# Performance work log

Measured on AMD Instinct MI355X. Metric: run time of the kernel, lower is better.

Reference implementation:

```python
import jax, jax.numpy as jnp
import numpy as np

AB = 8            # activation quant bits
NOISE_LEVEL = 0.1
CY_SCALE = 2.0    # stands in for args.cy_scale
B, IN, H = 8192, 512, 512


def _fake_quant(x, bits, sign):
    # forward: clip/clamp then round-to-grid; backward (STE) handled elsewhere
    if sign:
        delta = 1.0 / (2.0 ** (bits - 1))
        xc = jnp.clip(x, -1.0 + delta, 1.0 - delta)
        scale = 2.0 ** (bits - 1)
    else:
        xc = jnp.clip(x, 0.0, 1.0)
        scale = 2.0 ** bits
    q = jnp.round(xc * scale) / scale
    # STE: identity gradient w.r.t. x
    return x + jax.lax.stop_gradient(q - x)


def setup_inputs() -> dict:
    key = jax.random.key(0)
    ks = jax.random.split(key, 11)
    return {
        "input": jax.random.normal(ks[0], (B, IN), jnp.float32),
        "hx": jax.random.normal(ks[1], (B, H), jnp.float32),
        "cx": jax.random.normal(ks[2], (B, H), jnp.float32),
        "weight_ih": jax.random.normal(ks[3], (4 * H, IN), jnp.float32),
        "weight_hh": jax.random.normal(ks[4], (4 * H, H), jnp.float32),
        "bias_ih": jax.random.normal(ks[5], (4 * H,), jnp.float32),
        "bias_hh": jax.random.normal(ks[6], (4 * H,), jnp.float32),
        "noise_ih": jax.random.normal(ks[7], (IN, 4 * H), jnp.float32),
        "noise_hh": jax.random.normal(ks[8], (H, 4 * H), jnp.float32),
        "noise_bias_ih": jax.random.normal(ks[9], (4 * H,), jnp.float32),
        "noise_bias_hh": jax.random.normal(ks[10], (4 * H,), jnp.float32),
    }


def reference(input, hx, cx, weight_ih, weight_hh, bias_ih, bias_hh,
              noise_ih, noise_hh, noise_bias_ih, noise_bias_hh):
    # noisy weights: noise = randn * w.max() * noise_level (raw randn passed in)
    w_ih = weight_ih.T + noise_ih * (jnp.max(weight_ih) * NOISE_LEVEL)   # [IN,4H]
    w_hh = weight_hh.T + noise_hh * (jnp.max(weight_hh) * NOISE_LEVEL)   # [H,4H]
    b_ih = bias_ih + noise_bias_ih * (jnp.max(bias_ih) * NOISE_LEVEL)
    b_hh = bias_hh + noise_bias_hh * (jnp.max(bias_hh) * NOISE_LEVEL)

    gates = input @ w_ih + b_ih + hx @ w_hh + b_hh                        # [B,4H]
    ingate, forgetgate, cellgate, outgate = jnp.split(gates, 4, axis=1)

    ingate = _fake_quant(jax.nn.sigmoid(ingate), AB, False)
    forgetgate = _fake_quant(jax.nn.sigmoid(forgetgate), AB, False)
    cellgate = _fake_quant(jnp.tanh(cellgate), AB, True)
    outgate = _fake_quant(jax.nn.sigmoid(outgate), AB, False)

    cy = _fake_quant(
        (_fake_quant(forgetgate * cx, AB, True)
         + _fake_quant(ingate * cellgate, AB, True)) / CY_SCALE,
        AB, True)
    hy = _fake_quant(
        outgate * _fake_quant(jnp.tanh(cy * CY_SCALE), AB, True),
        AB, True)
    return (hy, cy)
```

## Files before the change

### kernel.cpp

```cpp
#include <hip/hip_runtime.h>
#include <cstdint>

typedef unsigned short u16;
typedef __bf16 bf16x8 __attribute__((ext_vector_type(8)));
typedef float f32x4 __attribute__((ext_vector_type(4)));

#define NB 8192
#define HD 512
#define KD 1024
#define ND 2048
#define HY_OFF (NB * HD)
#define NT 32

__device__ __forceinline__ u16 f2bf(float f) {
  unsigned u = __float_as_uint(f);
  u += 0x7FFFu + ((u >> 16) & 1u);
  return (u16)(u >> 16);
}
__device__ __forceinline__ float bf2f(u16 h) {
  return __uint_as_float(((unsigned)h) << 16);
}
__device__ __forceinline__ void atomicMaxF(float* a, float v) {
  if (v >= 0.f) atomicMax((int*)a, __float_as_int(v));
  else          atomicMin((unsigned int*)a, __float_as_uint(v));
}
__device__ __forceinline__ float fq_u(float x) {
  float xc = fminf(fmaxf(x, 0.0f), 1.0f);
  return rintf(xc * 256.0f) * (1.0f / 256.0f);
}
__device__ __forceinline__ float fq_s(float x) {
  const float lim = 1.0f - 1.0f / 128.0f;
  float xc = fminf(fmaxf(x, -lim), lim);
  return rintf(xc * 128.0f) * (1.0f / 128.0f);
}
__device__ __forceinline__ float sigm(float x) { return 1.0f / (1.0f + expf(-x)); }

__device__ __forceinline__ void gload_lds16(const u16* g, u16* l) {
  __builtin_amdgcn_global_load_lds(
      (const __attribute__((address_space(1))) void*)g,
      (__attribute__((address_space(3))) void*)l, 16, 0, 0);
}

__global__ __launch_bounds__(256) void k_prep_max(
    const float* __restrict__ w_ih, const float* __restrict__ w_hh,
    const float* __restrict__ b_ih, const float* __restrict__ b_hh,
    float* __restrict__ maxes) {
  int bid = blockIdx.x;
  const float* src; int slot, base;
  if (bid < 1024)      { src = w_ih; slot = 0; base = bid * 1024; }
  else if (bid < 2048) { src = w_hh; slot = 1; base = (bid - 1024) * 1024; }
  else if (bid < 2050) { src = b_ih; slot = 2; base = (bid - 2048) * 1024; }
  else                 { src = b_hh; slot = 3; base = (bid - 2050) * 1024; }
  float m = -INFINITY;
  for (int i = threadIdx.x; i < 1024; i += 256) m = fmaxf(m, src[base + i]);
  for (int k = 1; k < 64; k <<= 1) m = fmaxf(m, __shfl_xor(m, k, 64));
  __shared__ float sm[4];
  if ((threadIdx.x & 63) == 0) sm[threadIdx.x >> 6] = m;
  __syncthreads();
  if (threadIdx.x == 0) {
    m = fmaxf(fmaxf(sm[0], sm[1]), fmaxf(sm[2], sm[3]));
    atomicMaxF(&maxes[slot], m);
  }
}

__global__ __launch_bounds__(256) void k_prep_build(
    const float* __restrict__ input, const float* __restrict__ hx,
    const float* __restrict__ w_ih, const float* __restrict__ w_hh,
    const float* __restrict__ n_ih, const float* __restrict__ n_hh,
    const float* __restrict__ b_ih, const float* __restrict__ b_hh,
    const float* __restrict__ nb_ih, const float* __restrict__ nb_hh,
    const float* __restrict__ maxes,
    u16* __restrict__ Xhi, u16* __restrict__ Xlo,
    u16* __restrict__ Whi, u16* __restrict__ Wlo,
    float* __restrict__ biasC) {
  const int bid = blockIdx.x;
  if (bid < 2048) {
    const int total4 = NB * KD / 4;
    for (int e4 = bid * 256 + threadIdx.x; e4 < total4; e4 += 2048 * 256) {
      int row = e4 >> 8;
      int c4  = e4 & 255;
      float4 v = (c4 < 128)
          ? reinterpret_cast<const float4*>(input)[row * 128 + c4]
          : reinterpret_cast<const float4*>(hx)[row * 128 + (c4 - 128)];
      float xs[4] = {v.x, v.y, v.z, v.w};
      ushort4 hi, lo;
      u16 h0 = f2bf(xs[0]); u16 l0 = f2bf(xs[0] - bf2f(h0));
      u16 h1 = f2bf(xs[1]); u16 l1 = f2bf(xs[1] - bf2f(h1));
      u16 h2 = f2bf(xs[2]); u16 l2 = f2bf(xs[2] - bf2f(h2));
      u16 h3 = f2bf(xs[3]); u16 l3 = f2bf(xs[3] - bf2f(h3));
      hi.x = h0; hi.y = h1; hi.z = h2; hi.w = h3;
      lo.x = l0; lo.y = l1; lo.z = l2; lo.w = l3;
      reinterpret_cast<ushort4*>(Xhi)[e4] = hi;
      reinterpret_cast<ushort4*>(Xlo)[e4] = lo;
    }
  } else if (bid < 2560) {
    __shared__ float nT[256][17];
    const int w  = bid - 2048;
    const int cg = w >> 2, kb = w & 3;
    const int j0 = cg * 16;
    const int g  = ((j0 >> 7) & 1) * 2 + ((j0 >> 4) & 1);
    const int hb = ((j0 >> 8) << 2) | ((j0 >> 5) & 3);
    const int col0 = g * 512 + (hb << 4);
    const int k0 = kb * 256;
    {
      const int cl = threadIdx.x & 15;
      const int kr = threadIdx.x >> 4;
#pragma unroll 4
      for (int i = 0; i < 16; ++i) {
        const int k = k0 + kr + 16 * i;
        nT[kr + 16 * i][cl] = (k < 512) ? n_ih[k * ND + col0 + cl]
                                        : n_hh[(k - 512) * ND + col0 + cl];
      }
    }
    __syncthreads();
    const float s_ih = maxes[0] * 0.1f, s_hh = maxes[1] * 0.1f;
    const int c  = threadIdx.x >> 4;
    const int kl = threadIdx.x & 15;
    const int colL = col0 + c;
    const int j = j0 + c;
#pragma unroll
    for (int kk = 0; kk < 4; ++kk) {
      const int k = k0 + kk * 64 + kl * 4;
      float4 wv; float s;
      if (k < 512) {
        wv = reinterpret_cast<const float4*>(w_ih)[(colL * 512 + k) >> 2];
        s = s_ih;
      } else {
        wv = reinterpret_cast<const float4*>(w_hh)[(colL * 512 + k - 512) >> 2];
        s = s_hh;
      }
      const int kt = k - k0;
      float xs[4] = {wv.x + nT[kt + 0][c] * s, wv.y + nT[kt + 1][c] * s,
                     wv.z + nT[kt + 2][c] * s, wv.w + nT[kt + 3][c] * s};
      ushort4 hi, lo;
      u16 h0 = f2bf(xs[0]); u16 l0 = f2bf(xs[0] - bf2f(h0));
      u16 h1 = f2bf(xs[1]); u16 l1 = f2bf(xs[1] - bf2f(h1));
      u16 h2 = f2bf(xs[2]); u16 l2 = f2bf(xs[2] - bf2f(h2));
      u16 h3 = f2bf(xs[3]); u16 l3 = f2bf(xs[3] - bf2f(h3));
      hi.x = h0; hi.y = h1; hi.z = h2; hi.w = h3;
      lo.x = l0; lo.y = l1; lo.z = l2; lo.w = l3;
      reinterpret_cast<ushort4*>(Whi)[(j * KD + k) >> 2] = hi;
      reinterpret_cast<ushort4*>(Wlo)[(j * KD + k) >> 2] = lo;
    }
  } else {
    int j = (bid - 2560) * 256 + threadIdx.x;
    if (j < ND) {
      int g  = ((j >> 7) & 1) * 2 + ((j >> 4) & 1);
      int hb = ((j >> 8) << 2) | ((j >> 5) & 3);
      int col = g * 512 + (hb << 4) + (j & 15);
      biasC[j] = b_ih[col] + nb_ih[col] * (maxes[2] * 0.1f)
               + b_hh[col] + nb_hh[col] * (maxes[3] * 0.1f);
    }
  }
}

__global__ __launch_bounds__(512, 2) void k_gemm_lstm(
    const u16* __restrict__ Xhi, const u16* __restrict__ Xlo,
    const u16* __restrict__ Whi, const u16* __restrict__ Wlo,
    const float* __restrict__ biasC, const float* __restrict__ cx,
    float* __restrict__ out) {
  __shared__ u16 L[2][4][8192];
  const int tid  = threadIdx.x;
  const int lane = tid & 63, wid = tid >> 6;
  const int wr = wid >> 2, wc = wid & 3;
  const int lr = lane & 15, lg = lane >> 4;
  const int xcd = blockIdx.x & 7, tt = blockIdx.x >> 3;
  const int bm = ((xcd >> 1) << 3) | (tt & 7);
  const int bn = ((xcd & 1) << 2) | (tt >> 3);
  const int mbase = bm * 256, nbase = bn * 256;

  const int l8 = lane >> 3, l7 = lane & 7;
  const int csrc  = l7 ^ l8;
  const int srow  = wid * 16 + 2 * l8 + (csrc >> 2);
  const int skoff = (csrc & 3) * 8;
  const int sdst  = wid * 512;

  const int fro = (lr >> 1) * 64 + ((((lr & 1) << 2) | lg) ^ ((lr >> 1) & 7)) * 8;

  f32x4 acc[8][4] = {};
  bf16x8 afr[4][2];
  bf16x8 bfr[2][2][2];

#define STAGE(V, SLOT, BUF, HALF)                                             \
  {                                                                           \
    const u16* arr_ = (BUF) == 0 ? Xhi : (BUF) == 1 ? Xlo                     \
                      : (BUF) == 2 ? Whi : Wlo;                               \
    const int gb_ = ((BUF) < 2 ? mbase : nbase) + (HALF) * 128 + srow;        \
    gload_lds16(arr_ + (size_t)gb_ * KD + (V) * 32 + skoff,                   \
                &L[(SLOT)][(BUF)][(HALF) * 4096 + sdst]);                     \
  }

#define PH(S, MH, NH, LOADA, LOADB, STAGE_CODE, WAIT_CODE)                    \
  {                                                                           \
    if (LOADA) {                                                              \
      _Pragma("unroll") for (int m2 = 0; m2 < 4; ++m2) {                      \
        const int ab = ((MH) * 128 + wr * 64 + m2 * 16) * 32 + fro;           \
        afr[m2][0] = *reinterpret_cast<const bf16x8*>(&L[S][0][ab]);          \
        afr[m2][1] = *reinterpret_cast<const bf16x8*>(&L[S][1][ab]);          \
      }                                                                       \
    }                                                                         \
    if (LOADB) {                                                              \
      _Pragma("unroll") for (int n2 = 0; n2 < 2; ++n2) {                      \
        const int bb = ((NH) * 128 + wc * 32 + n2 * 16) * 32 + fro;           \
        bfr[(NH)][n2][0] = *reinterpret_cast<const bf16x8*>(&L[S][2][bb]);    \
        bfr[(NH)][n2][1] = *reinterpret_cast<const bf16x8*>(&L[S][3][bb]);    \
      }                                                                       \
    }                                                                         \
    STAGE_CODE;                                                               \
    WAIT_CODE;                                                                \
    __builtin_amdgcn_s_barrier();                                             \
    __builtin_amdgcn_s_setprio(1);                                            \
    _Pragma("unroll") for (int t = 0; t < 3; ++t)                             \
      _Pragma("unroll") for (int m2 = 0; m2 < 4; ++m2)                        \
        _Pragma("unroll") for (int n2 = 0; n2 < 2; ++n2) {                    \
          f32x4* ac = &acc[(MH) * 4 + m2][(NH) * 2 + n2];                     \
          *ac = __builtin_amdgcn_mfma_f32_16x16x32_bf16(afr[m2][t == 1],      \
                    bfr[(NH)][n2][t == 2], *ac, 0, 0, 0);                     \
        }                                                                     \
    __builtin_amdgcn_s_setprio(0);                                            \
    __builtin_amdgcn_s_barrier();                                             \
  }

#define V6 asm volatile("s_waitcnt vmcnt(6)" ::: "memory")
#define V0 asm volatile("s_waitcnt vmcnt(0)" ::: "memory")

#define TILE(U, S)                                                            \
  PH(S, 0, 0, 1, 1,                                                           \
     { STAGE((U) + 1, (S) ^ 1, 0, 1); STAGE((U) + 1, (S) ^ 1, 1, 1); }, )     \
  PH(S, 0, 1, 0, 1,                                                           \
     { STAGE((U) + 2, (S), 0, 0); STAGE((U) + 2, (S), 1, 0); }, )             \
  PH(S, 1, 1, 1, 0,                                                           \
     { STAGE((U) + 2, (S), 2, 0); STAGE((U) + 2, (S), 3, 0); }, )             \
  PH(S, 1, 0, 0, 0,                                                           \
     { STAGE((U) + 2, (S), 2, 1); STAGE((U) + 2, (S), 3, 1); }, V6)

  STAGE(0, 0, 0, 0); STAGE(0, 0, 1, 0);
  STAGE(0, 0, 2, 0); STAGE(0, 0, 3, 0);
  STAGE(0, 0, 2, 1); STAGE(0, 0, 3, 1);
  STAGE(0, 0, 0, 1); STAGE(0, 0, 1, 1);
  STAGE(1, 1, 0, 0); STAGE(1, 1, 1, 0);
  STAGE(1, 1, 2, 0); STAGE(1, 1, 3, 0);
  STAGE(1, 1, 2, 1); STAGE(1, 1, 3, 1);
  V6;
  __builtin_amdgcn_s_barrier();

  for (int u = 0; u < NT - 4; u += 2) {
    TILE(u, 0)
    TILE(u + 1, 1)
  }
  TILE(NT - 4, 0)
  TILE(NT - 3, 1)
  PH(0, 0, 0, 1, 1, { STAGE(31, 1, 0, 1); STAGE(31, 1, 1, 1); }, )
  PH(0, 0, 1, 0, 1, , )
  PH(0, 1, 1, 1, 0, , )
  PH(0, 1, 0, 0, 0, , V0)
  PH(1, 0, 0, 1, 1, , )
  PH(1, 0, 1, 0, 1, , )
  PH(1, 1, 1, 1, 0, , )
  PH(1, 1, 0, 0, 0, , )

#undef TILE
#undef V6
#undef V0
#undef PH
#undef STAGE

  const int hb = bn * 4 + wc;
  const int h = hb * 16 + lr;
  float bias[4];
#pragma unroll
  for (int g = 0; g < 4; ++g)
    bias[g] = biasC[bn * 256 + ((g >> 1) * 8 + wc * 2 + (g & 1)) * 16 + lr];
#pragma unroll
  for (int mh = 0; mh < 2; ++mh) {
#pragma unroll
    for (int m2 = 0; m2 < 4; ++m2) {
      const int m = mh * 4 + m2;
#pragma unroll
      for (int r = 0; r < 4; ++r) {
        const int row = mbase + mh * 128 + wr * 64 + m2 * 16 + lg * 4 + r;
        const float gi = acc[m][0][r] + bias[0];
        const float gf = acc[m][1][r] + bias[1];
        const float gc = acc[m][2][r] + bias[2];
        const float go = acc[m][3][r] + bias[3];
        const float ig = fq_u(sigm(gi));
        const float fg = fq_u(sigm(gf));
        const float cg = fq_s(tanhf(gc));
        const float og = fq_u(sigm(go));
        const float cxv = cx[(size_t)row * HD + h];
        const float t1 = fq_s(fg * cxv);
        const float t2 = fq_s(ig * cg);
        const float cyv = fq_s((t1 + t2) * 0.5f);
        const float hyv = fq_s(og * fq_s(tanhf(cyv * 2.0f)));
        out[(size_t)row * HD + h] = hyv;
        out[HY_OFF + (size_t)row * HD + h] = cyv;
      }
    }
  }
}

extern "C" void kernel_launch(void* const* d_in, const int* in_sizes, int n_in,
                              void* d_out, int out_size, void* d_ws, size_t ws_size,
                              hipStream_t stream) {
  const float* input = (const float*)d_in[0];
  const float* hx    = (const float*)d_in[1];
  const float* cx    = (const float*)d_in[2];
  const float* w_ih  = (const float*)d_in[3];
  const float* w_hh  = (const float*)d_in[4];
  const float* b_ih  = (const float*)d_in[5];
  const float* b_hh  = (const float*)d_in[6];
  const float* n_ih  = (const float*)d_in[7];
  const float* n_hh  = (const float*)d_in[8];
  const float* nb_ih = (const float*)d_in[9];
  const float* nb_hh = (const float*)d_in[10];
  float* out = (float*)d_out;

  char* ws = (char*)d_ws;
  float* maxes = (float*)ws;
  u16* Xhi = (u16*)(ws + 256);
  u16* Xlo = (u16*)(ws + 256 + 16777216);
  u16* Whi = (u16*)(ws + 256 + 2 * 16777216);
  u16* Wlo = (u16*)(ws + 256 + 2 * 16777216 + 4194304);
  float* biasC = (float*)(ws + 256 + 2 * 16777216 + 2 * 4194304);

  hipMemsetAsync(maxes, 0xFF, 16, stream);
  hipLaunchKernelGGL(k_prep_max, dim3(2052), dim3(256), 0, stream,
                     w_ih, w_hh, b_ih, b_hh, maxes);
  hipLaunchKernelGGL(k_prep_build, dim3(2568), dim3(256), 0, stream,
                     input, hx, w_ih, w_hh, n_ih, n_hh, b_ih, b_hh,
                     nb_ih, nb_hh, maxes, Xhi, Xlo, Whi, Wlo, biasC);
  hipLaunchKernelGGL(k_gemm_lstm, dim3(256), dim3(512), 0, stream,
                     Xhi, Xlo, Whi, Wlo, biasC, cx, out);
}
```

Measured before the change: 146.4 us.

## Double-buffer LDS fragment registers to prefetch next phase operands during MFMA

Splits the A/B register fragments into two ping-pong sets and issues LDS reads for the next phase's operands (including the next K-tile's A half) before the barrier of the current phase, so LDS read latency overlaps with MFMA work. Adds sched_barrier fences to keep the compiler from reordering, moves the vmcnt wait to a different phase with a tighter count, and restructures the loop tail accordingly. This raises register pressure and changes wait timing, which could reduce occupancy or create hazards if the wait points are wrong.

```diff
diff --git a/kernel.cpp b/kernel.cpp
--- a/kernel.cpp
+++ b/kernel.cpp
@@ -178,8 +178,10 @@
   const int fro = (lr >> 1) * 64 + ((((lr & 1) << 2) | lg) ^ ((lr >> 1) & 7)) * 8;
 
   f32x4 acc[8][4] = {};
-  bf16x8 afr[4][2];
-  bf16x8 bfr[2][2][2];
+  bf16x8 afr0[4][2];
+  bf16x8 afr1[4][2];
+  bf16x8 bfr0[2][2];
+  bf16x8 bfr1[2][2];
 
 #define STAGE(V, SLOT, BUF, HALF)                                             \
   {                                                                           \
@@ -190,49 +192,54 @@
                 &L[(SLOT)][(BUF)][(HALF) * 4096 + sdst]);                     \
   }
 
-#define PH(S, MH, NH, LOADA, LOADB, STAGE_CODE, WAIT_CODE)                    \
+#define RD_A(DST, S, MH)                                                      \
+  _Pragma("unroll") for (int m2 = 0; m2 < 4; ++m2) {                          \
+    const int ab = ((MH) * 128 + wr * 64 + m2 * 16) * 32 + fro;               \
+    DST[m2][0] = *reinterpret_cast<const bf16x8*>(&L[S][0][ab]);              \
+    DST[m2][1] = *reinterpret_cast<const bf16x8*>(&L[S][1][ab]);              \
+  }
+
+#define RD_B(DST, S, NH)                                                      \
+  _Pragma("unroll") for (int n2 = 0; n2 < 2; ++n2) {                          \
+    const int bb = ((NH) * 128 + wc * 32 + n2 * 16) * 32 + fro;               \
+    DST[n2][0] = *reinterpret_cast<const bf16x8*>(&L[S][2][bb]);              \
+    DST[n2][1] = *reinterpret_cast<const bf16x8*>(&L[S][3][bb]);              \
+  }
+
+#define PH(MH, NH, AARR, BARR, STAGE_CODE, READ_CODE, WAIT_CODE)              \
   {                                                                           \
-    if (LOADA) {                                                              \
-      _Pragma("unroll") for (int m2 = 0; m2 < 4; ++m2) {                      \
-        const int ab = ((MH) * 128 + wr * 64 + m2 * 16) * 32 + fro;           \
-        afr[m2][0] = *reinterpret_cast<const bf16x8*>(&L[S][0][ab]);          \
-        afr[m2][1] = *reinterpret_cast<const bf16x8*>(&L[S][1][ab]);          \
-      }                                                                       \
-    }                                                                         \
-    if (LOADB) {                                                              \
-      _Pragma("unroll") for (int n2 = 0; n2 < 2; ++n2) {                      \
-        const int bb = ((NH) * 128 + wc * 32 + n2 * 16) * 32 + fro;           \
-        bfr[(NH)][n2][0] = *reinterpret_cast<const bf16x8*>(&L[S][2][bb]);    \
-        bfr[(NH)][n2][1] = *reinterpret_cast<const bf16x8*>(&L[S][3][bb]);    \
-      }                                                                       \
-    }                                                                         \
     STAGE_CODE;                                                               \
+    READ_CODE;                                                                \
     WAIT_CODE;                                                                \
+    __builtin_amdgcn_sched_barrier(0);                                        \
     __builtin_amdgcn_s_barrier();                                             \
     __builtin_amdgcn_s_setprio(1);                                            \
     _Pragma("unroll") for (int t = 0; t < 3; ++t)                             \
       _Pragma("unroll") for (int m2 = 0; m2 < 4; ++m2)                        \
         _Pragma("unroll") for (int n2 = 0; n2 < 2; ++n2) {                    \
           f32x4* ac = &acc[(MH) * 4 + m2][(NH) * 2 + n2];                     \
-          *ac = __builtin_amdgcn_mfma_f32_16x16x32_bf16(afr[m2][t == 1],      \
-                    bfr[(NH)][n2][t == 2], *ac, 0, 0, 0);                     \
+          *ac = __builtin_amdgcn_mfma_f32_16x16x32_bf16(AARR[m2][t == 1],     \
+                    BARR[n2][t == 2], *ac, 0, 0, 0);                          \
         }                                                                     \
     __builtin_amdgcn_s_setprio(0);                                            \
     __builtin_amdgcn_s_barrier();                                             \
   }
 
-#define V6 asm volatile("s_waitcnt vmcnt(6)" ::: "memory")
+#define V4 asm volatile("s_waitcnt vmcnt(4)" ::: "memory")
 #define V0 asm volatile("s_waitcnt vmcnt(0)" ::: "memory")
 
 #define TILE(U, S)                                                            \
-  PH(S, 0, 0, 1, 1,                                                           \
-     { STAGE((U) + 1, (S) ^ 1, 0, 1); STAGE((U) + 1, (S) ^ 1, 1, 1); }, )     \
-  PH(S, 0, 1, 0, 1,                                                           \
-     { STAGE((U) + 2, (S), 0, 0); STAGE((U) + 2, (S), 1, 0); }, )             \
-  PH(S, 1, 1, 1, 0,                                                           \
-     { STAGE((U) + 2, (S), 2, 0); STAGE((U) + 2, (S), 3, 0); }, )             \
-  PH(S, 1, 0, 0, 0,                                                           \
-     { STAGE((U) + 2, (S), 2, 1); STAGE((U) + 2, (S), 3, 1); }, V6)
+  PH(0, 0, afr0, bfr0,                                                        \
+     { STAGE((U) + 1, (S) ^ 1, 0, 1); STAGE((U) + 1, (S) ^ 1, 1, 1); },       \
+     { RD_B(bfr0, S, 0); RD_B(bfr1, S, 1); }, )                               \
+  PH(0, 1, afr0, bfr1,                                                        \
+     { STAGE((U) + 2, (S), 0, 0); STAGE((U) + 2, (S), 1, 0); },               \
+     { RD_A(afr1, S, 1); }, )                                                 \
+  PH(1, 1, afr1, bfr1,                                                        \
+     { STAGE((U) + 2, (S), 2, 0); STAGE((U) + 2, (S), 3, 0); }, , V4)         \
+  PH(1, 0, afr1, bfr0,                                                        \
+     { STAGE((U) + 2, (S), 2, 1); STAGE((U) + 2, (S), 3, 1); },               \
+     { RD_A(afr0, (S) ^ 1, 0); }, )
 
   STAGE(0, 0, 0, 0); STAGE(0, 0, 1, 0);
   STAGE(0, 0, 2, 0); STAGE(0, 0, 3, 0);
@@ -241,28 +248,32 @@
   STAGE(1, 1, 0, 0); STAGE(1, 1, 1, 0);
   STAGE(1, 1, 2, 0); STAGE(1, 1, 3, 0);
   STAGE(1, 1, 2, 1); STAGE(1, 1, 3, 1);
-  V6;
+  asm volatile("s_waitcnt vmcnt(6)" ::: "memory");
   __builtin_amdgcn_s_barrier();
-
-  for (int u = 0; u < NT - 4; u += 2) {
+  RD_A(afr0, 0, 0);
+  __builtin_amdgcn_sched_barrier(0);
+
+  for (int u = 0; u < NT - 2; u += 2) {
     TILE(u, 0)
     TILE(u + 1, 1)
   }
-  TILE(NT - 4, 0)
-  TILE(NT - 3, 1)
-  PH(0, 0, 0, 1, 1, { STAGE(31, 1, 0, 1); STAGE(31, 1, 1, 1); }, )
-  PH(0, 0, 1, 0, 1, , )
-  PH(0, 1, 1, 1, 0, , )
-  PH(0, 1, 0, 0, 0, , V0)
-  PH(1, 0, 0, 1, 1, , )
-  PH(1, 0, 1, 0, 1, , )
-  PH(1, 1, 1, 1, 0, , )
-  PH(1, 1, 0, 0, 0, , )
+  PH(0, 0, afr0, bfr0,
+     { STAGE(31, 1, 0, 1); STAGE(31, 1, 1, 1); },
+     { RD_B(bfr0, 0, 0); RD_B(bfr1, 0, 1); }, )
+  PH(0, 1, afr0, bfr1, , { RD_A(afr1, 0, 1); }, )
+  PH(1, 1, afr1, bfr1, , , V0)
+  PH(1, 0, afr1, bfr0, , { RD_A(afr0, 1, 0); }, )
+  PH(0, 0, afr0, bfr0, , { RD_B(bfr0, 1, 0); RD_B(bfr1, 1, 1); }, )
+  PH(0, 1, afr0, bfr1, , { RD_A(afr1, 1, 1); }, )
+  PH(1, 1, afr1, bfr1, , , )
+  PH(1, 0, afr1, bfr0, , , )
 
 #undef TILE
-#undef V6
+#undef V4
 #undef V0
 #undef PH
+#undef RD_A
+#undef RD_B
 #undef STAGE
 
   const int hb = bn * 4 + wc;
```

After: 190.7 us. 1.3x slower.

## Replace fine-grained 8-phase LDS pipeline with simple double-buffered tile loop

Applied to the files above, without the earlier changes.

Replaces the interleaved per-phase staging, two barriers per phase and manual vmcnt waits with a simple double buffer. The whole next K-tile is issued at tile start, four MFMA phases run, then one __syncthreads per tile. This cuts barrier count and scheduling complexity but loses the deeper prefetch distance and fine overlap of global loads with MFMA work. It may expose more memory latency.

```diff
diff --git a/kernel.cpp b/kernel.cpp
--- a/kernel.cpp
+++ b/kernel.cpp
@@ -190,7 +190,15 @@
                 &L[(SLOT)][(BUF)][(HALF) * 4096 + sdst]);                     \
   }
 
-#define PH(S, MH, NH, LOADA, LOADB, STAGE_CODE, WAIT_CODE)                    \
+#define STAGE8(V, SLOT)                                                       \
+  {                                                                           \
+    STAGE(V, SLOT, 0, 0); STAGE(V, SLOT, 1, 0);                               \
+    STAGE(V, SLOT, 2, 0); STAGE(V, SLOT, 3, 0);                               \
+    STAGE(V, SLOT, 2, 1); STAGE(V, SLOT, 3, 1);                               \
+    STAGE(V, SLOT, 0, 1); STAGE(V, SLOT, 1, 1);                               \
+  }
+
+#define PHX(S, MH, NH, LOADA, LOADB)                                          \
   {                                                                           \
     if (LOADA) {                                                              \
       _Pragma("unroll") for (int m2 = 0; m2 < 4; ++m2) {                      \
@@ -206,9 +214,6 @@
         bfr[(NH)][n2][1] = *reinterpret_cast<const bf16x8*>(&L[S][3][bb]);    \
       }                                                                       \
     }                                                                         \
-    STAGE_CODE;                                                               \
-    WAIT_CODE;                                                                \
-    __builtin_amdgcn_s_barrier();                                             \
     __builtin_amdgcn_s_setprio(1);                                            \
     _Pragma("unroll") for (int t = 0; t < 3; ++t)                             \
       _Pragma("unroll") for (int m2 = 0; m2 < 4; ++m2)                        \
@@ -218,51 +223,32 @@
                     bfr[(NH)][n2][t == 2], *ac, 0, 0, 0);                     \
         }                                                                     \
     __builtin_amdgcn_s_setprio(0);                                            \
-    __builtin_amdgcn_s_barrier();                                             \
-  }
-
-#define V6 asm volatile("s_waitcnt vmcnt(6)" ::: "memory")
-#define V0 asm volatile("s_waitcnt vmcnt(0)" ::: "memory")
+  }
 
 #define TILE(U, S)                                                            \
-  PH(S, 0, 0, 1, 1,                                                           \
-     { STAGE((U) + 1, (S) ^ 1, 0, 1); STAGE((U) + 1, (S) ^ 1, 1, 1); }, )     \
-  PH(S, 0, 1, 0, 1,                                                           \
-     { STAGE((U) + 2, (S), 0, 0); STAGE((U) + 2, (S), 1, 0); }, )             \
-  PH(S, 1, 1, 1, 0,                                                           \
-     { STAGE((U) + 2, (S), 2, 0); STAGE((U) + 2, (S), 3, 0); }, )             \
-  PH(S, 1, 0, 0, 0,                                                           \
-     { STAGE((U) + 2, (S), 2, 1); STAGE((U) + 2, (S), 3, 1); }, V6)
-
-  STAGE(0, 0, 0, 0); STAGE(0, 0, 1, 0);
-  STAGE(0, 0, 2, 0); STAGE(0, 0, 3, 0);
-  STAGE(0, 0, 2, 1); STAGE(0, 0, 3, 1);
-  STAGE(0, 0, 0, 1); STAGE(0, 0, 1, 1);
-  STAGE(1, 1, 0, 0); STAGE(1, 1, 1, 0);
-  STAGE(1, 1, 2, 0); STAGE(1, 1, 3, 0);
-  STAGE(1, 1, 2, 1); STAGE(1, 1, 3, 1);
-  V6;
-  __builtin_amdgcn_s_barrier();
-
-  for (int u = 0; u < NT - 4; u += 2) {
+  STAGE8((U) + 1, (S) ^ 1)                                                    \
+  PHX(S, 0, 0, 1, 1)                                                          \
+  PHX(S, 0, 1, 0, 1)                                                          \
+  PHX(S, 1, 1, 1, 0)                                                          \
+  PHX(S, 1, 0, 0, 0)                                                          \
+  __syncthreads();
+
+  STAGE8(0, 0)
+  __syncthreads();
+
+  for (int u = 0; u < NT - 2; u += 2) {
     TILE(u, 0)
     TILE(u + 1, 1)
   }
-  TILE(NT - 4, 0)
-  TILE(NT - 3, 1)
-  PH(0, 0, 0, 1, 1, { STAGE(31, 1, 0, 1); STAGE(31, 1, 1, 1); }, )
-  PH(0, 0, 1, 0, 1, , )
-  PH(0, 1, 1, 1, 0, , )
-  PH(0, 1, 0, 0, 0, , V0)
-  PH(1, 0, 0, 1, 1, , )
-  PH(1, 0, 1, 0, 1, , )
-  PH(1, 1, 1, 1, 0, , )
-  PH(1, 1, 0, 0, 0, , )
+  TILE(30, 0)
+  PHX(1, 0, 0, 1, 1)
+  PHX(1, 0, 1, 0, 1)
+  PHX(1, 1, 1, 1, 0)
+  PHX(1, 1, 0, 0, 0)
 
 #undef TILE
-#undef V6
-#undef V0
-#undef PH
+#undef PHX
+#undef STAGE8
 #undef STAGE
 
   const int hb = bn * 4 + wc;
```

Result: slower. 149.7 us (+2.3%).
